# Performance work log

Hardware: AMD Instinct MI355X
Metric: run time of the kernel (lower is better)

Reference implementation:

```python
import jax, jax.numpy as jnp
import numpy as np

ALPHA = 100.0   # norse SuperSpike surrogate-gradient sharpness (default)
DT = 0.001      # norse LIFBoxParameters default dt

@jax.custom_vjp
def heaviside(x):
    # spike function with SuperSpike surrogate gradient (norse method='super')
    return (x > 0).astype(x.dtype)

def _hs_fwd(x):
    return (x > 0).astype(x.dtype), x

def _hs_bwd(x, g):
    return (g / (ALPHA * jnp.abs(x) + 1.0) ** 2,)

heaviside.defvjp(_hs_fwd, _hs_bwd)


def setup_inputs() -> dict:
    key = jax.random.key(0)
    k0, k1, k2, k3, k4 = jax.random.split(key, 5)
    B, F, T = 256, 10, 8192
    inputs = jax.random.normal(k0, (B, F, T), dtype=jnp.float32)
    # learned scalar LIF parameters (one per parallel temporal layer)
    tau = jnp.array([200.0, 300.0, 600.0], dtype=jnp.float32)   # tau_mem_inv
    v_th = jnp.array([0.006, 0.008, 0.013], dtype=jnp.float32)  # thresholds
    conv_w = jax.random.normal(k1, (1, 3, 1, 1), dtype=jnp.float32) * 0.5
    conv_b = jax.random.normal(k2, (1,), dtype=jnp.float32) * 0.1
    lin_w = jax.random.normal(k3, (2, 10), dtype=jnp.float32) * 0.3
    lin_b = jax.random.normal(k4, (2,), dtype=jnp.float32) * 0.1
    return {"inputs": inputs, "tau": tau, "v_th": v_th,
            "conv_w": conv_w, "conv_b": conv_b, "lin_w": lin_w, "lin_b": lin_b}


def reference(inputs, tau, v_th, conv_w, conv_b, lin_w, lin_b):
    # inputs: [B, F, T]
    B, F, T = inputs.shape
    x_t = jnp.transpose(inputs, (2, 0, 1))          # [T, B, F], time-major
    tau3 = tau[:, None, None]                        # [3,1,1] broadcast over B,F
    vth3 = v_th[:, None, None]
    v0 = jnp.zeros((3, B, F), dtype=inputs.dtype)    # v_leak = 0 initial state

    def step(v, x):
        # LIFBox dynamics: dv = dt * tau_inv * (v_leak - v + i), v_leak=v_reset=0
        v = v + DT * tau3 * (x[None, :, :] - v)      # [3,B,F]
        z = heaviside(v - vth3)                      # spikes
        v = (1.0 - z) * v                            # reset to v_reset=0 on spike
        return v, z

    _, zs = jax.lax.scan(step, v0, x_t)              # zs: [T, 3, B, F]
    resp = jnp.transpose(zs, (2, 1, 3, 0))           # [B, 3, F, T]

    # 1x1 Conv2d over the 3 LIF channels -> [B, F, T]
    conv = jnp.einsum('bcft,c->bft', resp, conv_w[0, :, 0, 0]) + conv_b[0]
    # Linear over feature dim F=10 -> 2, output [B, 2, T]
    out = jnp.einsum('bft,of->bot', conv, lin_w) + lin_b[None, :, None]
    return out
```

## Files before the change

kernel.cpp:

```cpp
#include <hip/hip_runtime.h>


#define T_LEN 8192
#define NF 10
#define NSEQ 30
#define CHUNK 256
#define WARM 128
#define NCHUNKS 32
#define NWIN 12
#define WWIN 4
#define NROW 20
#define BUF4 (NROW * 8)

__device__ __forceinline__ float lif_step(float xx, float v, float k, float vt, bool& s) {
  float d  = __fsub_rn(xx, v);
  float p  = __fmul_rn(k, d);
  float vn = __fadd_rn(v, p);
  s = vn > vt;
  return s ? 0.0f : vn;
}

__device__ __forceinline__ float lut_sum(unsigned m, const float* lut, int o, float bias) {
  float acc = bias;
#pragma unroll
  for (int g = 0; g < 6; ++g) {
    unsigned val = (m >> (5 * g)) & 31u;
    acc += lut[(g * 2 + o) * 32 + val];
  }
  return acc;
}

#define STEP_CAP(XX, T)                                            \
  {                                                                \
    bool s;                                                        \
    v = lif_step((XX), v, k, vt, s);                               \
    unsigned long long ub = __ballot(s);                           \
    if (tt == (T)) {                                               \
      mA = (unsigned)(ub & 0xffffffffull);                         \
      mB = (unsigned)(ub >> 32);                                   \
    }                                                              \
  }

__global__ __launch_bounds__(64, 4) void lif_chunked(
    const float* __restrict__ x,
    const float* __restrict__ tau,
    const float* __restrict__ vth,
    const float* __restrict__ convw,
    const float* __restrict__ convb,
    const float* __restrict__ linw,
    const float* __restrict__ linb,
    float* __restrict__ out)
{
  const int b    = blockIdx.x;
  const int cb   = blockIdx.y;
  const int lane = threadIdx.x;
  const int half = lane >> 5;
  const int j    = lane & 31;
  const bool active = j < NSEQ;
  const int c = active ? j / NF : 0;
  const int f = active ? j % NF : 0;

  __shared__ float lut[384];
  __shared__ float4 xbuf[3][BUF4];
#pragma unroll
  for (int e = 0; e < 6; ++e) {
    int id = lane + 64 * e;
    int g = id >> 6, rem = id & 63, oo = rem >> 5, val = rem & 31;
    float sacc = 0.0f;
#pragma unroll
    for (int p = 0; p < 5; ++p) {
      if (val & (1 << p)) {
        int jj = 5 * g + p;
        sacc += convw[jj / NF] * linw[oo * NF + (jj % NF)];
      }
    }
    lut[id] = sacc;
  }
  __syncthreads();

  const float k  = __fmul_rn(0.001f, tau[c]);
  const float vt = active ? vth[c] : 3.0e38f;
  const int chunk = cb * 2 + half;

  const int srow = half * NF + f;
  const int sw   = srow & 7;

  const int id0 = lane,        id1 = lane + 64,  id2 = (lane & 31) + 128;
  const int row0 = id0 >> 3,   row1 = id1 >> 3,  row2 = id2 >> 3;
  const int q0 = id0 & 7,      q1 = id1 & 7,     q2 = id2 & 7;
  const int ch0 = 2 * cb + row0 / NF, ch1 = 2 * cb + row1 / NF, ch2 = 2 * cb + row2 / NF;
  const int fr0 = row0 % NF,   fr1 = row1 % NF,  fr2 = row2 % NF;
  const int ts0 = (ch0 == 0) ? 0 : ch0 * CHUNK - WARM;
  const int ts1 = (ch1 == 0) ? 0 : ch1 * CHUNK - WARM;
  const int ts2 = (ch2 == 0) ? 0 : ch2 * CHUNK - WARM;
  const float4* gp0 = (const float4*)(x + ((size_t)b * NF + fr0) * (size_t)T_LEN + ts0) + q0;
  const float4* gp1 = (const float4*)(x + ((size_t)b * NF + fr1) * (size_t)T_LEN + ts1) + q1;
  const float4* gp2 = (const float4*)(x + ((size_t)b * NF + fr2) * (size_t)T_LEN + ts2) + q2;
  const int lpo0 = row0 * 8 + (q0 ^ (row0 & 7));
  const int lpo1 = row1 * 8 + (q1 ^ (row1 & 7));
  const int lpo2 = row2 * 8 + (q2 ^ (row2 & 7));
  const int adj0 = (ch0 == 0) ? -(WARM / 4) : 0;
  const int adj1 = (ch1 == 0) ? -(WARM / 4) : 0;
  const int adj2 = (ch2 == 0) ? -(WARM / 4) : 0;

  const int o  = half;
  const int tt = j;
  float wsum = 0.0f;
#pragma unroll
  for (int f2 = 0; f2 < NF; ++f2) wsum += linw[o * NF + f2];
  const float bias = linb[o] + convb[0] * wsum;

  const int tA = 2 * cb * CHUNK;
  float* outA = out + ((size_t)b * 2 + o) * T_LEN + tA;
  float* outB = outA + CHUNK;

  float4 rA0 = gp0[0], rA1 = gp1[0], rA2 = gp2[0];
  gp0 += 8; gp1 += 8; gp2 += 8;
  {
    float4* wp = &xbuf[0][0];
    wp[lpo0] = rA0; wp[lpo1] = rA1; wp[lpo2] = rA2;
  }
  rA0 = gp0[0]; rA1 = gp1[0]; rA2 = gp2[0];
  gp0 += 8; gp1 += 8; gp2 += 8;

  float v = 0.0f;

#pragma unroll 1
  for (int w = 0; w < NWIN; ++w) {
    float4 rB0, rB1, rB2;
    const bool issueNext = (w + 2 < NWIN);
    if (issueNext) {
      if (w + 2 == WWIN) { gp0 += adj0; gp1 += adj1; gp2 += adj2; }
      rB0 = gp0[0]; rB1 = gp1[0]; rB2 = gp2[0];
      gp0 += 8; gp1 += 8; gp2 += 8;
    }

    const float4* rp = &xbuf[w % 3][srow * 8];
    unsigned mA = 0, mB = 0;
    float4 x0 = rp[0 ^ sw];
    float4 x1 = rp[1 ^ sw];
#pragma unroll
    for (int q = 0; q < 8; ++q) {
      float4 xn = x1;
      if (q + 2 < 8) xn = rp[(q + 2) ^ sw];
      STEP_CAP(x0.x, 4 * q + 0)
      STEP_CAP(x0.y, 4 * q + 1)
      STEP_CAP(x0.z, 4 * q + 2)
      STEP_CAP(x0.w, 4 * q + 3)
      x0 = x1; x1 = xn;
    }

    if (w >= WWIN) {
      const int ow = w - WWIN;
      outA[ow * 32 + tt] = lut_sum(mA, lut, o, bias);
      outB[ow * 32 + tt] = lut_sum(mB, lut, o, bias);
    }
    if (w == WWIN - 1) v = (chunk == 0) ? 0.0f : v;

    if (w + 1 < NWIN) {
      float4* wp = &xbuf[(w + 1) % 3][0];
      wp[lpo0] = rA0; wp[lpo1] = rA1; wp[lpo2] = rA2;
    }
    rA0 = rB0; rA1 = rB1; rA2 = rB2;
  }
}

extern "C" void kernel_launch(void* const* d_in, const int* in_sizes, int n_in,
                              void* d_out, int out_size, void* d_ws, size_t ws_size,
                              hipStream_t stream) {
  const float* x     = (const float*)d_in[0];
  const float* tau   = (const float*)d_in[1];
  const float* vthp  = (const float*)d_in[2];
  const float* convw = (const float*)d_in[3];
  const float* convb = (const float*)d_in[4];
  const float* linw  = (const float*)d_in[5];
  const float* linb  = (const float*)d_in[6];
  float* out = (float*)d_out;

  const int B = in_sizes[0] / (NF * T_LEN);
  lif_chunked<<<dim3(B, NCHUNKS / 2), dim3(64), 0, stream>>>(
      x, tau, vthp, convw, convb, linw, linb, out);
}
```

Before: 151.5 us.

## Split warmup and output loops, double-buffer LDS, and rebalance output writes

```diff
diff --git a/kernel.cpp b/kernel.cpp
--- a/kernel.cpp
+++ b/kernel.cpp
@@ -30,15 +30,12 @@
   return acc;
 }
 
-#define STEP_CAP(XX, T)                                            \
-  {                                                                \
-    bool s;                                                        \
-    v = lif_step((XX), v, k, vt, s);                               \
-    unsigned long long ub = __ballot(s);                           \
-    if (tt == (T)) {                                               \
-      mA = (unsigned)(ub & 0xffffffffull);                         \
-      mB = (unsigned)(ub >> 32);                                   \
-    }                                                              \
+#define STEP_CAP(XX, T)                                \
+  {                                                    \
+    bool s;                                            \
+    v = lif_step((XX), v, k, vt, s);                   \
+    unsigned long long ub = __ballot(s);               \
+    uM = (tt == (T)) ? ub : uM;                        \
   }
 
 __global__ __launch_bounds__(64, 4) void lif_chunked(
@@ -61,7 +58,7 @@
   const int f = active ? j % NF : 0;
 
   __shared__ float lut[384];
-  __shared__ float4 xbuf[3][BUF4];
+  __shared__ float4 xbuf[2][BUF4];
 #pragma unroll
   for (int e = 0; e < 6; ++e) {
     int id = lane + 64 * e;
@@ -82,8 +79,9 @@
   const float vt = active ? vth[c] : 3.0e38f;
   const int chunk = cb * 2 + half;
 
-  const int srow = half * NF + f;
-  const int sw   = srow & 7;
+  const int srow  = half * NF + f;
+  const char* sbase = (const char*)&xbuf[0][0];
+  const int rbyte = srow * 128 + (srow & 7) * 16;
 
   const int id0 = lane,        id1 = lane + 64,  id2 = (lane & 31) + 128;
   const int row0 = id0 >> 3,   row1 = id1 >> 3,  row2 = id2 >> 3;
@@ -103,46 +101,69 @@
   const int adj1 = (ch1 == 0) ? -(WARM / 4) : 0;
   const int adj2 = (ch2 == 0) ? -(WARM / 4) : 0;
 
-  const int o  = half;
   const int tt = j;
-  float wsum = 0.0f;
-#pragma unroll
-  for (int f2 = 0; f2 < NF; ++f2) wsum += linw[o * NF + f2];
-  const float bias = linb[o] + convb[0] * wsum;
-
-  const int tA = 2 * cb * CHUNK;
-  float* outA = out + ((size_t)b * 2 + o) * T_LEN + tA;
-  float* outB = outA + CHUNK;
-
-  float4 rA0 = gp0[0], rA1 = gp1[0], rA2 = gp2[0];
-  gp0 += 8; gp1 += 8; gp2 += 8;
+  float wsum0 = 0.0f, wsum1 = 0.0f;
+#pragma unroll
+  for (int f2 = 0; f2 < NF; ++f2) { wsum0 += linw[f2]; wsum1 += linw[NF + f2]; }
+  const float bias0 = linb[0] + convb[0] * wsum0;
+  const float bias1 = linb[1] + convb[0] * wsum1;
+
+  const int tH = chunk * CHUNK;
+  float* out0 = out + ((size_t)b * 2 + 0) * T_LEN + tH;
+  float* out1 = out + ((size_t)b * 2 + 1) * T_LEN + tH;
+
   {
+    float4 s0 = gp0[0], s1 = gp1[0], s2 = gp2[0];
+    gp0 += 8; gp1 += 8; gp2 += 8;
     float4* wp = &xbuf[0][0];
-    wp[lpo0] = rA0; wp[lpo1] = rA1; wp[lpo2] = rA2;
-  }
-  rA0 = gp0[0]; rA1 = gp1[0]; rA2 = gp2[0];
-  gp0 += 8; gp1 += 8; gp2 += 8;
+    wp[lpo0] = s0; wp[lpo1] = s1; wp[lpo2] = s2;
+  }
 
   float v = 0.0f;
 
 #pragma unroll 1
-  for (int w = 0; w < NWIN; ++w) {
-    float4 rB0, rB1, rB2;
-    const bool issueNext = (w + 2 < NWIN);
-    if (issueNext) {
-      if (w + 2 == WWIN) { gp0 += adj0; gp1 += adj1; gp2 += adj2; }
-      rB0 = gp0[0]; rB1 = gp1[0]; rB2 = gp2[0];
-      gp0 += 8; gp1 += 8; gp2 += 8;
-    }
-
-    const float4* rp = &xbuf[w % 3][srow * 8];
-    unsigned mA = 0, mB = 0;
-    float4 x0 = rp[0 ^ sw];
-    float4 x1 = rp[1 ^ sw];
+  for (int w = 0; w < WWIN; ++w) {
+    if (w + 1 == WWIN) { gp0 += adj0; gp1 += adj1; gp2 += adj2; }
+    float4 rN0 = gp0[0], rN1 = gp1[0], rN2 = gp2[0];
+    gp0 += 8; gp1 += 8; gp2 += 8;
+
+    const int wb = rbyte + (w & 1) * (BUF4 * 16);
+    float4 x0 = *(const float4*)(sbase + (wb ^ 0));
+    float4 x1 = *(const float4*)(sbase + (wb ^ 16));
 #pragma unroll
     for (int q = 0; q < 8; ++q) {
       float4 xn = x1;
-      if (q + 2 < 8) xn = rp[(q + 2) ^ sw];
+      if (q + 2 < 8) xn = *(const float4*)(sbase + (wb ^ ((q + 2) << 4)));
+      bool s;
+      v = lif_step(x0.x, v, k, vt, s);
+      v = lif_step(x0.y, v, k, vt, s);
+      v = lif_step(x0.z, v, k, vt, s);
+      v = lif_step(x0.w, v, k, vt, s);
+      x0 = x1; x1 = xn;
+    }
+
+    float4* wp = &xbuf[(w + 1) & 1][0];
+    wp[lpo0] = rN0; wp[lpo1] = rN1; wp[lpo2] = rN2;
+  }
+  v = (chunk == 0) ? 0.0f : v;
+
+#pragma unroll 1
+  for (int w = WWIN; w < NWIN; ++w) {
+    float4 rN0, rN1, rN2;
+    const bool haveNext = (w + 1 < NWIN);
+    if (haveNext) {
+      rN0 = gp0[0]; rN1 = gp1[0]; rN2 = gp2[0];
+      gp0 += 8; gp1 += 8; gp2 += 8;
+    }
+
+    unsigned long long uM = 0;
+    const int wb = rbyte + (w & 1) * (BUF4 * 16);
+    float4 x0 = *(const float4*)(sbase + (wb ^ 0));
+    float4 x1 = *(const float4*)(sbase + (wb ^ 16));
+#pragma unroll
+    for (int q = 0; q < 8; ++q) {
+      float4 xn = x1;
+      if (q + 2 < 8) xn = *(const float4*)(sbase + (wb ^ ((q + 2) << 4)));
       STEP_CAP(x0.x, 4 * q + 0)
       STEP_CAP(x0.y, 4 * q + 1)
       STEP_CAP(x0.z, 4 * q + 2)
@@ -150,18 +171,15 @@
       x0 = x1; x1 = xn;
     }
 
-    if (w >= WWIN) {
-      const int ow = w - WWIN;
-      outA[ow * 32 + tt] = lut_sum(mA, lut, o, bias);
-      outB[ow * 32 + tt] = lut_sum(mB, lut, o, bias);
-    }
-    if (w == WWIN - 1) v = (chunk == 0) ? 0.0f : v;
-
-    if (w + 1 < NWIN) {
-      float4* wp = &xbuf[(w + 1) % 3][0];
-      wp[lpo0] = rA0; wp[lpo1] = rA1; wp[lpo2] = rA2;
-    }
-    rA0 = rB0; rA1 = rB1; rA2 = rB2;
+    const unsigned vM = half ? (unsigned)(uM >> 32) : (unsigned)uM;
+    const int ow = w - WWIN;
+    out0[ow * 32 + tt] = lut_sum(vM, lut, 0, bias0);
+    out1[ow * 32 + tt] = lut_sum(vM, lut, 1, bias1);
+
+    if (haveNext) {
+      float4* wp = &xbuf[(w + 1) & 1][0];
+      wp[lpo0] = rN0; wp[lpo1] = rN1; wp[lpo2] = rN2;
+    }
   }
 }
 
```

Result: faster. 146.5 us (-3.3%).
